# Kernel tuning notes

Hardware: AMD Instinct MI355X
Metric: run time of the kernel (lower is better)

Reference implementation:

```python
import jax, jax.numpy as jnp
import numpy as np

NUM_HEADS = 16
WINDOW = 256


def setup_inputs() -> dict:
    key = jax.random.key(0)
    ks = jax.random.split(key, 9)
    B, S, H = 2, 2048, 1024
    sc = 0.02
    return {
        "hidden_states": jax.random.normal(ks[0], (B, S, H), jnp.float32),
        "wq": jax.random.normal(ks[1], (H, H), jnp.float32) * sc,
        "bq": jax.random.normal(ks[2], (H,), jnp.float32) * sc,
        "wk": jax.random.normal(ks[3], (H, H), jnp.float32) * sc,
        "bk": jax.random.normal(ks[4], (H,), jnp.float32) * sc,
        "wv": jax.random.normal(ks[5], (H, H), jnp.float32) * sc,
        "bv": jax.random.normal(ks[6], (H,), jnp.float32) * sc,
        "wo": jax.random.normal(ks[7], (H, H), jnp.float32) * sc,
        "bo": jax.random.normal(ks[8], (H,), jnp.float32) * sc,
    }


def reference(hidden_states, wq, bq, wk, bk, wv, bv, wo, bo):
    B, S, H = hidden_states.shape
    nH, hd = NUM_HEADS, H // NUM_HEADS
    scale = 1.0 / np.sqrt(hd).astype(np.float32)

    def heads(x):  # [B,S,H] -> [B,nH,S,hd]
        return x.reshape(B, S, nH, hd).transpose(0, 2, 1, 3)

    q = heads(hidden_states @ wq.T + bq)
    k = heads(hidden_states @ wk.T + bk)
    v = heads(hidden_states @ wv.T + bv)

    scores = jnp.einsum("bhqd,bhkd->bhqk", q, k) * scale  # [B,nH,S,S]

    # allowed keys for query i: j in [i - WINDOW, i] (causal window)
    i = jnp.arange(S)[:, None]
    j = jnp.arange(S)[None, :]
    allowed = (j <= i) & (j >= i - WINDOW)  # [S,S]

    scores = jnp.where(allowed[None, None], scores, -jnp.inf)
    # original clamps AFTER masking -> -inf becomes -10000 (soft mask)
    scores = jnp.clip(scores, -10000.0, 10000.0)

    probs = jax.nn.softmax(scores, axis=-1)
    probs = jnp.nan_to_num(probs, nan=0.0, posinf=0.0, neginf=0.0)

    out = jnp.einsum("bhqk,bhkd->bhqd", probs, v)  # [B,nH,S,hd]
    out = out.transpose(0, 2, 1, 3).reshape(B, S, H)
    return out @ wo.T + bo
```

## Files before the change

### kernel.cpp

```cpp
#include <hip/hip_runtime.h>
#include <hip/hip_bf16.h>
#include <stdint.h>

typedef __attribute__((ext_vector_type(8))) short short8;
typedef __attribute__((ext_vector_type(4))) float f32x4;
typedef __attribute__((ext_vector_type(4))) unsigned short u16x4;

__device__ __forceinline__ float bf2f(unsigned short u) {
  union { unsigned int u; float f; } x; x.u = ((unsigned int)u) << 16; return x.f;
}
__device__ __forceinline__ unsigned short f2bf(float f) {
  union { float f; unsigned int u; } x; x.f = f;
  unsigned int u = x.u;
  return (unsigned short)((u + 0x7fffu + ((u >> 16) & 1u)) >> 16);
}

__device__ __forceinline__ void gload_lds16(const void* g, void* l) {
  __builtin_amdgcn_global_load_lds(
      (const __attribute__((address_space(1))) void*)g,
      (__attribute__((address_space(3))) void*)l, 16, 0, 0);
}

__global__ void cvt4(const float* __restrict__ s, unsigned short* __restrict__ d) {
  int i = (blockIdx.x * 256 + threadIdx.x) * 4;
  f32x4 f = *(const f32x4*)(s + i);
  u16x4 o = { f2bf(f[0]), f2bf(f[1]), f2bf(f[2]), f2bf(f[3]) };
  *(u16x4*)(d + i) = o;
}

__global__ void cvt_w(const float* __restrict__ w0, const float* __restrict__ w1,
                      const float* __restrict__ w2, const float* __restrict__ w3,
                      unsigned short* __restrict__ dst) {
  const float* s = blockIdx.z == 0 ? w0 : blockIdx.z == 1 ? w1 : blockIdx.z == 2 ? w2 : w3;
  unsigned short* d = dst + (size_t)blockIdx.z * 1048576;
  int i = (blockIdx.x * 256 + threadIdx.x) * 4;
  f32x4 f = *(const f32x4*)(s + i);
  u16x4 o = { f2bf(f[0]), f2bf(f[1]), f2bf(f[2]), f2bf(f[3]) };
  *(u16x4*)(d + i) = o;
}

template <int MODE>
__global__ __launch_bounds__(256)
void gemm_bt(const unsigned short* __restrict__ A,
             const unsigned short* __restrict__ Wbase,
             const float* __restrict__ b0, const float* __restrict__ b1,
             const float* __restrict__ b2,
             unsigned short* __restrict__ obf, float* __restrict__ of32) {
  const int K = 1024, NT = 32;
  const int z = blockIdx.z;
  const unsigned short* W = Wbase + (size_t)z * 1048576;
  const float* bias = (z == 0) ? b0 : (z == 1) ? b1 : b2;

  int flat = blockIdx.y * 8 + blockIdx.x;
  int swz = (flat & 7) * 32 + (flat >> 3);
  const int n0 = (swz & 7) * 128, m0 = (swz >> 3) * 128;

  const int tid = threadIdx.x, lane = tid & 63, w = tid >> 6;
  const int wr = w >> 1, wc = w & 1;
  const int fr = lane & 15, g = lane >> 4;

  __shared__ unsigned short lds[3][8192];

  f32x4 acc[4][4] = {};

#define STAGE(bi, t)                                                            \
  do {                                                                          \
    _Pragma("unroll") for (int i = 0; i < 2; ++i) {                             \
      int s = i * 256 + tid;                                                    \
      int row = s >> 2;                                                         \
      int gc = (s & 3) ^ ((row >> 1) & 3);                                      \
      gload_lds16(A + (size_t)(m0 + row) * K + (t) * 32 + gc * 8,               \
                  &lds[bi][s * 8]);                                             \
      gload_lds16(W + (size_t)(n0 + row) * K + (t) * 32 + gc * 8,               \
                  &lds[bi][4096 + s * 8]);                                      \
    }                                                                           \
  } while (0)

#define COMPUTE(bi)                                                             \
  do {                                                                          \
    short8 af[4], bfr[4];                                                       \
    _Pragma("unroll") for (int m = 0; m < 4; ++m) {                             \
      int ra = wr * 64 + m * 16 + fr;                                           \
      af[m] = *(const short8*)&lds[bi][ra * 32 + ((g ^ ((ra >> 1) & 3)) * 8)];  \
    }                                                                           \
    _Pragma("unroll") for (int n = 0; n < 4; ++n) {                             \
      int rb2 = wc * 64 + n * 16 + fr;                                          \
      bfr[n] =                                                                  \
          *(const short8*)&lds[bi][4096 + rb2 * 32 + ((g ^ ((rb2 >> 1) & 3)) * 8)]; \
    }                                                                           \
    _Pragma("unroll") for (int m = 0; m < 4; ++m)                               \
        _Pragma("unroll") for (int n = 0; n < 4; ++n)                           \
        acc[m][n] = __builtin_amdgcn_mfma_f32_16x16x32_bf16(af[m], bfr[n],      \
                                                            acc[m][n], 0, 0, 0);\
  } while (0)

  STAGE(0, 0);
  STAGE(1, 1);
  for (int t = 0; t < NT; ++t) {
    if (t < NT - 1)
      asm volatile("s_waitcnt vmcnt(4)" ::: "memory");
    else
      asm volatile("s_waitcnt vmcnt(0)" ::: "memory");
    __builtin_amdgcn_s_barrier();
    __builtin_amdgcn_sched_barrier(0);
    if (t + 2 < NT) STAGE((t + 2) % 3, t + 2);
    __builtin_amdgcn_s_setprio(1);
    COMPUTE(t % 3);
    __builtin_amdgcn_s_setprio(0);
  }
#undef STAGE
#undef COMPUTE

  const int rb = g * 4, cl = fr;
#pragma unroll
  for (int m = 0; m < 4; ++m) {
#pragma unroll
    for (int n = 0; n < 4; ++n) {
      int col = n0 + wc * 64 + n * 16 + cl;
      float bias_v = bias[col];
      int row0 = m0 + wr * 64 + m * 16 + rb;
      if (MODE == 0) {
        int hh = col >> 6, d = col & 63;
        int bb = row0 >> 11, s0 = row0 & 2047;
        if (z == 2) {
          u16x4 pk;
#pragma unroll
          for (int i = 0; i < 4; ++i) pk[i] = f2bf(acc[m][n][i] + bias_v);
          *(u16x4*)&obf[(((size_t)(64 + bb * 16 + hh)) * 64 + d) * 2048 + s0] = pk;
        } else {
#pragma unroll
          for (int i = 0; i < 4; ++i)
            obf[(((size_t)(z * 32 + bb * 16 + hh)) * 2048 + s0 + i) * 64 + d] =
                f2bf(acc[m][n][i] + bias_v);
        }
      } else {
#pragma unroll
        for (int i = 0; i < 4; ++i)
          of32[(size_t)(row0 + i) * 1024 + col] = acc[m][n][i] + bias_v;
      }
    }
  }
}

__global__ __launch_bounds__(256)
void attn_mfma(const unsigned short* __restrict__ QKV, unsigned short* __restrict__ AO) {
  const int S = 2048;
  const int b = blockIdx.z, h = blockIdx.y;
  const int q0 = blockIdx.x * 128;
  const size_t hb = (size_t)(b * 16 + h);
  const unsigned short* Qh = QKV + hb * (S * 64);
  const unsigned short* Kh = QKV + 4194304 + hb * (S * 64);
  const unsigned short* Vt = QKV + 8388608 + hb * (S * 64);

  const int tid = threadIdx.x;
  const int lane = tid & 63, w = tid >> 6;
  const int c = lane & 15, g = lane >> 4;
  const int qw0 = q0 + 32 * w;

  __shared__ unsigned short Plds[4][1024];
  char* Pb = (char*)&Plds[w][0];

  short8 qa[2][2];
#pragma unroll
  for (int mi = 0; mi < 2; ++mi)
#pragma unroll
    for (int cs = 0; cs < 2; ++cs)
      qa[mi][cs] = *(const short8*)(Qh + (size_t)(qw0 + 16 * mi + c) * 64 + 32 * cs + g * 8);

  f32x4 o[2][4] = {};
  float mrow[2][4], lsum[2][4];
#pragma unroll
  for (int mi = 0; mi < 2; ++mi)
#pragma unroll
    for (int r = 0; r < 4; ++r) { mrow[mi][r] = -1e30f; lsum[mi][r] = 0.f; }

  int kt0 = qw0 - 256; if (kt0 < 0) kt0 = 0;
  const int ktlast = qw0;

  short8 kf[2][2], vf[4];
#pragma unroll
  for (int ni = 0; ni < 2; ++ni)
#pragma unroll
    for (int cs = 0; cs < 2; ++cs)
      kf[ni][cs] = *(const short8*)(Kh + (size_t)(kt0 + 16 * ni + c) * 64 + 32 * cs + g * 8);
#pragma unroll
  for (int ni = 0; ni < 4; ++ni)
    vf[ni] = *(const short8*)(Vt + (size_t)(16 * ni + c) * 2048 + kt0 + g * 8);

  for (int kt = kt0; kt <= ktlast; kt += 32) {
    const int ktn = (kt + 32 <= ktlast) ? kt + 32 : kt;
    short8 kfn[2][2], vfn[4];
#pragma unroll
    for (int ni = 0; ni < 2; ++ni)
#pragma unroll
      for (int cs = 0; cs < 2; ++cs)
        kfn[ni][cs] = *(const short8*)(Kh + (size_t)(ktn + 16 * ni + c) * 64 + 32 * cs + g * 8);
#pragma unroll
    for (int ni = 0; ni < 4; ++ni)
      vfn[ni] = *(const short8*)(Vt + (size_t)(16 * ni + c) * 2048 + ktn + g * 8);

    f32x4 sA[2][2] = {};
#pragma unroll
    for (int mi = 0; mi < 2; ++mi)
#pragma unroll
      for (int ni = 0; ni < 2; ++ni)
#pragma unroll
        for (int cs = 0; cs < 2; ++cs)
          sA[mi][ni] = __builtin_amdgcn_mfma_f32_16x16x32_bf16(qa[mi][cs], kf[ni][cs],
                                                               sA[mi][ni], 0, 0, 0);

    float sv[2][2][4];
#pragma unroll
    for (int mi = 0; mi < 2; ++mi)
#pragma unroll
      for (int ni = 0; ni < 2; ++ni)
#pragma unroll
        for (int r = 0; r < 4; ++r) {
          int q = qw0 + 16 * mi + 4 * g + r;
          int k = kt + 16 * ni + c;
          sv[mi][ni][r] = ((unsigned)(q - k) <= 256u) ? sA[mi][ni][r] * 0.125f : -3.0e38f;
        }

#pragma unroll
    for (int mi = 0; mi < 2; ++mi) {
#pragma unroll
      for (int r = 0; r < 4; ++r) {
        float tm = fmaxf(sv[mi][0][r], sv[mi][1][r]);
        tm = fmaxf(tm, __shfl_xor(tm, 1));
        tm = fmaxf(tm, __shfl_xor(tm, 2));
        tm = fmaxf(tm, __shfl_xor(tm, 4));
        tm = fmaxf(tm, __shfl_xor(tm, 8));
        float mnew = fmaxf(mrow[mi][r], tm);
        float sc = __expf(mrow[mi][r] - mnew);
        mrow[mi][r] = mnew;
        float p0 = __expf(sv[mi][0][r] - mnew);
        float p1 = __expf(sv[mi][1][r] - mnew);
        float ps = p0 + p1;
        ps += __shfl_xor(ps, 1);
        ps += __shfl_xor(ps, 2);
        ps += __shfl_xor(ps, 4);
        ps += __shfl_xor(ps, 8);
        lsum[mi][r] = lsum[mi][r] * sc + ps;
#pragma unroll
        for (int ni = 0; ni < 4; ++ni)
          o[mi][ni][r] *= sc;
        int qloc = 16 * mi + 4 * g + r;
        int xr = (qloc & 12) << 2;
        *(unsigned short*)(Pb + ((qloc * 64 + c * 2) ^ xr)) = f2bf(p0);
        *(unsigned short*)(Pb + ((qloc * 64 + 32 + c * 2) ^ xr)) = f2bf(p1);
      }
    }

#pragma unroll
    for (int mi = 0; mi < 2; ++mi) {
      int qloc = 16 * mi + c;
      short8 pa = *(const short8*)(Pb + ((qloc * 64 + g * 16) ^ ((qloc & 12) << 2)));
#pragma unroll
      for (int ni = 0; ni < 4; ++ni)
        o[mi][ni] = __builtin_amdgcn_mfma_f32_16x16x32_bf16(pa, vf[ni], o[mi][ni], 0, 0, 0);
    }

#pragma unroll
    for (int ni = 0; ni < 2; ++ni)
#pragma unroll
      for (int cs = 0; cs < 2; ++cs)
        kf[ni][cs] = kfn[ni][cs];
#pragma unroll
    for (int ni = 0; ni < 4; ++ni)
      vf[ni] = vfn[ni];
  }

#pragma unroll
  for (int mi = 0; mi < 2; ++mi)
#pragma unroll
    for (int r = 0; r < 4; ++r) {
      float inv = 1.f / lsum[mi][r];
      int q = qw0 + 16 * mi + 4 * g + r;
      unsigned short* row = AO + (size_t)(b * 2048 + q) * 1024 + h * 64 + c;
#pragma unroll
      for (int ni = 0; ni < 4; ++ni)
        row[16 * ni] = f2bf(o[mi][ni][r] * inv);
    }
}

extern "C" void kernel_launch(void* const* d_in, const int* in_sizes, int n_in,
                              void* d_out, int out_size, void* d_ws, size_t ws_size,
                              hipStream_t stream) {
  const float* X  = (const float*)d_in[0];
  const float* wq = (const float*)d_in[1];
  const float* bq = (const float*)d_in[2];
  const float* wk = (const float*)d_in[3];
  const float* bk = (const float*)d_in[4];
  const float* wv = (const float*)d_in[5];
  const float* bv = (const float*)d_in[6];
  const float* wo = (const float*)d_in[7];
  const float* bo = (const float*)d_in[8];
  float* out = (float*)d_out;

  unsigned short* Xb  = (unsigned short*)d_ws;
  unsigned short* Wb  = Xb + 4194304;
  unsigned short* QKV = Wb + 4194304;
  unsigned short* AO  = QKV + 12582912;

  cvt4<<<dim3(4096), dim3(256), 0, stream>>>(X, Xb);
  cvt_w<<<dim3(1024, 1, 4), dim3(256), 0, stream>>>(wq, wk, wv, wo, Wb);
  gemm_bt<0><<<dim3(8, 32, 3), dim3(256), 0, stream>>>(Xb, Wb, bq, bk, bv, QKV, nullptr);
  attn_mfma<<<dim3(16, 16, 2), dim3(256), 0, stream>>>(QKV, AO);
  gemm_bt<1><<<dim3(8, 32, 1), dim3(256), 0, stream>>>(AO, Wb + 3 * 1048576, bo, bo, bo, nullptr, out);
}
```

Before: 92.94 us.

## Swap MFMA operands for vectorized epilogue stores; split QKV GEMM; narrower out-proj tiles

The GEMM kernel gains a SWAP mode that swaps the MFMA operand order, so each lane holds four consecutive output columns and can write them with one vector store (u16x4 for Q/K, f32x4 for the output projection) instead of four scattered scalar stores. The QKV projection is split into two launches: Q/K use the swapped path, and V keeps the transposed layout it needs. The output projection switches to 128x64 tiles with twice as many workgroups to fill more CUs, which changes the vmcnt wait counts. The cost is an extra kernel launch, and the smaller tiles give less data reuse per workgroup.

Result: slower. 98.57 us (+6.1%).

```diff
diff --git a/kernel.cpp b/kernel.cpp
--- a/kernel.cpp
+++ b/kernel.cpp
@@ -39,29 +39,38 @@
   *(u16x4*)(d + i) = o;
 }
 
-template <int MODE>
+template <int MODE, bool SWAP, int BN>
 __global__ __launch_bounds__(256)
 void gemm_bt(const unsigned short* __restrict__ A,
              const unsigned short* __restrict__ Wbase,
-             const float* __restrict__ b0, const float* __restrict__ b1,
-             const float* __restrict__ b2,
+             const float* __restrict__ bias0, const float* __restrict__ bias1,
              unsigned short* __restrict__ obf, float* __restrict__ of32) {
   const int K = 1024, NT = 32;
-  const int z = blockIdx.z;
-  const unsigned short* W = Wbase + (size_t)z * 1048576;
-  const float* bias = (z == 0) ? b0 : (z == 1) ? b1 : b2;
-
-  int flat = blockIdx.y * 8 + blockIdx.x;
-  int swz = (flat & 7) * 32 + (flat >> 3);
-  const int n0 = (swz & 7) * 128, m0 = (swz >> 3) * 128;
+  constexpr int GX = 1024 / BN;
+  constexpr int LB = BN / 64;
+  constexpr int NWC = BN / 64;
+  constexpr int NWR = 4 / NWC;
+  constexpr int MS = 128 / NWR;
+  constexpr int MR = MS / 16;
+  constexpr int ASZ = 128 * 32, BSZ = BN * 32;
+
+  const int z = (MODE == 0 && SWAP) ? blockIdx.z : 2;
+  const unsigned short* W =
+      (MODE == 0 && SWAP) ? Wbase + ((size_t)blockIdx.z << 20) : Wbase;
+  const float* bias = (MODE == 0 && SWAP && blockIdx.z == 1) ? bias1 : bias0;
+
+  constexpr int NWG = GX * 32;
+  int flat = blockIdx.y * GX + blockIdx.x;
+  int swz = (flat & 7) * (NWG / 8) + (flat >> 3);
+  const int n0 = (swz % GX) * BN, m0 = (swz / GX) * 128;
 
   const int tid = threadIdx.x, lane = tid & 63, w = tid >> 6;
-  const int wr = w >> 1, wc = w & 1;
+  const int wr = w / NWC, wc = w % NWC;
   const int fr = lane & 15, g = lane >> 4;
 
-  __shared__ unsigned short lds[3][8192];
-
-  f32x4 acc[4][4] = {};
+  __shared__ unsigned short lds[3][ASZ + BSZ];
+
+  f32x4 acc[MR][4] = {};
 
 #define STAGE(bi, t)                                                            \
   do {                                                                          \
@@ -71,36 +80,50 @@
       int gc = (s & 3) ^ ((row >> 1) & 3);                                      \
       gload_lds16(A + (size_t)(m0 + row) * K + (t) * 32 + gc * 8,               \
                   &lds[bi][s * 8]);                                             \
+    }                                                                           \
+    _Pragma("unroll") for (int i = 0; i < LB; ++i) {                            \
+      int s = i * 256 + tid;                                                    \
+      int row = s >> 2;                                                         \
+      int gc = (s & 3) ^ ((row >> 1) & 3);                                      \
       gload_lds16(W + (size_t)(n0 + row) * K + (t) * 32 + gc * 8,               \
-                  &lds[bi][4096 + s * 8]);                                      \
+                  &lds[bi][ASZ + s * 8]);                                       \
     }                                                                           \
   } while (0)
 
 #define COMPUTE(bi)                                                             \
   do {                                                                          \
-    short8 af[4], bfr[4];                                                       \
-    _Pragma("unroll") for (int m = 0; m < 4; ++m) {                             \
-      int ra = wr * 64 + m * 16 + fr;                                           \
+    short8 af[MR], bfr[4];                                                      \
+    _Pragma("unroll") for (int m = 0; m < MR; ++m) {                            \
+      int ra = wr * MS + m * 16 + fr;                                           \
       af[m] = *(const short8*)&lds[bi][ra * 32 + ((g ^ ((ra >> 1) & 3)) * 8)];  \
     }                                                                           \
     _Pragma("unroll") for (int n = 0; n < 4; ++n) {                             \
       int rb2 = wc * 64 + n * 16 + fr;                                          \
-      bfr[n] =                                                                  \
-          *(const short8*)&lds[bi][4096 + rb2 * 32 + ((g ^ ((rb2 >> 1) & 3)) * 8)]; \
-    }                                                                           \
-    _Pragma("unroll") for (int m = 0; m < 4; ++m)                               \
-        _Pragma("unroll") for (int n = 0; n < 4; ++n)                           \
+      bfr[n] = *(const short8*)&lds[bi][ASZ + rb2 * 32 +                        \
+                                        ((g ^ ((rb2 >> 1) & 3)) * 8)];          \
+    }                                                                           \
+    _Pragma("unroll") for (int m = 0; m < MR; ++m)                              \
+        _Pragma("unroll") for (int n = 0; n < 4; ++n) {                         \
+      if constexpr (SWAP)                                                       \
+        acc[m][n] = __builtin_amdgcn_mfma_f32_16x16x32_bf16(bfr[n], af[m],      \
+                                                            acc[m][n], 0, 0, 0);\
+      else                                                                      \
         acc[m][n] = __builtin_amdgcn_mfma_f32_16x16x32_bf16(af[m], bfr[n],      \
                                                             acc[m][n], 0, 0, 0);\
+    }                                                                           \
   } while (0)
 
   STAGE(0, 0);
   STAGE(1, 1);
   for (int t = 0; t < NT; ++t) {
-    if (t < NT - 1)
-      asm volatile("s_waitcnt vmcnt(4)" ::: "memory");
-    else
+    if (t < NT - 1) {
+      if constexpr (BN == 128)
+        asm volatile("s_waitcnt vmcnt(4)" ::: "memory");
+      else
+        asm volatile("s_waitcnt vmcnt(3)" ::: "memory");
+    } else {
       asm volatile("s_waitcnt vmcnt(0)" ::: "memory");
+    }
     __builtin_amdgcn_s_barrier();
     __builtin_amdgcn_sched_barrier(0);
     if (t + 2 < NT) STAGE((t + 2) % 3, t + 2);
@@ -111,32 +134,43 @@
 #undef STAGE
 #undef COMPUTE
 
-  const int rb = g * 4, cl = fr;
-#pragma unroll
-  for (int m = 0; m < 4; ++m) {
-#pragma unroll
-    for (int n = 0; n < 4; ++n) {
-      int col = n0 + wc * 64 + n * 16 + cl;
-      float bias_v = bias[col];
-      int row0 = m0 + wr * 64 + m * 16 + rb;
-      if (MODE == 0) {
+  if constexpr (SWAP) {
+#pragma unroll
+    for (int m = 0; m < MR; ++m) {
+#pragma unroll
+      for (int n = 0; n < 4; ++n) {
+        int token = m0 + wr * MS + m * 16 + fr;
+        int col0 = n0 + wc * 64 + n * 16 + g * 4;
+        f32x4 bv = *(const f32x4*)&bias[col0];
+        if (MODE == 0) {
+          u16x4 pk;
+#pragma unroll
+          for (int i = 0; i < 4; ++i) pk[i] = f2bf(acc[m][n][i] + bv[i]);
+          int hh = col0 >> 6, d0 = col0 & 63;
+          int bb = token >> 11, s0 = token & 2047;
+          *(u16x4*)&obf[(((size_t)(z * 32 + bb * 16 + hh)) * 2048 + s0) * 64 + d0] = pk;
+        } else {
+          f32x4 o;
+#pragma unroll
+          for (int i = 0; i < 4; ++i) o[i] = acc[m][n][i] + bv[i];
+          *(f32x4*)&of32[(size_t)token * 1024 + col0] = o;
+        }
+      }
+    }
+  } else {
+#pragma unroll
+    for (int m = 0; m < MR; ++m) {
+#pragma unroll
+      for (int n = 0; n < 4; ++n) {
+        int col = n0 + wc * 64 + n * 16 + fr;
+        float bias_v = bias[col];
+        int row0 = m0 + wr * MS + m * 16 + g * 4;
         int hh = col >> 6, d = col & 63;
         int bb = row0 >> 11, s0 = row0 & 2047;
-        if (z == 2) {
-          u16x4 pk;
-#pragma unroll
-          for (int i = 0; i < 4; ++i) pk[i] = f2bf(acc[m][n][i] + bias_v);
-          *(u16x4*)&obf[(((size_t)(64 + bb * 16 + hh)) * 64 + d) * 2048 + s0] = pk;
-        } else {
-#pragma unroll
-          for (int i = 0; i < 4; ++i)
-            obf[(((size_t)(z * 32 + bb * 16 + hh)) * 2048 + s0 + i) * 64 + d] =
-                f2bf(acc[m][n][i] + bias_v);
-        }
-      } else {
-#pragma unroll
-        for (int i = 0; i < 4; ++i)
-          of32[(size_t)(row0 + i) * 1024 + col] = acc[m][n][i] + bias_v;
+        u16x4 pk;
+#pragma unroll
+        for (int i = 0; i < 4; ++i) pk[i] = f2bf(acc[m][n][i] + bias_v);
+        *(u16x4*)&obf[(((size_t)(64 + bb * 16 + hh)) * 64 + d) * 2048 + s0] = pk;
       }
     }
   }
@@ -304,7 +338,11 @@
 
   cvt4<<<dim3(4096), dim3(256), 0, stream>>>(X, Xb);
   cvt_w<<<dim3(1024, 1, 4), dim3(256), 0, stream>>>(wq, wk, wv, wo, Wb);
-  gemm_bt<0><<<dim3(8, 32, 3), dim3(256), 0, stream>>>(Xb, Wb, bq, bk, bv, QKV, nullptr);
+  gemm_bt<0, true, 128><<<dim3(8, 32, 2), dim3(256), 0, stream>>>(
+      Xb, Wb, bq, bk, QKV, nullptr);
+  gemm_bt<0, false, 128><<<dim3(8, 32, 1), dim3(256), 0, stream>>>(
+      Xb, Wb + 2 * 1048576, bv, bv, QKV, nullptr);
   attn_mfma<<<dim3(16, 16, 2), dim3(256), 0, stream>>>(QKV, AO);
-  gemm_bt<1><<<dim3(8, 32, 1), dim3(256), 0, stream>>>(AO, Wb + 3 * 1048576, bo, bo, bo, nullptr, out);
-}
+  gemm_bt<1, true, 64><<<dim3(16, 32, 1), dim3(256), 0, stream>>>(
+      AO, Wb + 3 * 1048576, bo, bo, nullptr, out);
+}
```
